# Kernel tuning notes

Measured on AMD Instinct MI355X. Metric: run time of the kernel, lower is better.

Reference implementation:

```python
import jax, jax.numpy as jnp
import numpy as np

# DCE-MRI protocol constants (config values in original repo)
TR = 0.005                      # repetition time (s)
ALPHA = 15.0 / 180.0 * np.pi    # flip angle (rad)
DELTT = 4.5 / 60.0              # temporal resolution (min)
R1_RELAX = 4.5                  # contrast agent relaxivity
SIN_A = float(np.sin(ALPHA))
COS_A = float(np.cos(ALPHA))

B = 262144
T = 112


def setup_inputs() -> dict:
    key = jax.random.key(0)
    k1, k2, k3 = jax.random.split(key, 3)
    param = jax.random.uniform(k1, (B, 3), dtype=jnp.float32)
    T10 = jax.random.uniform(k2, (B, 1), dtype=jnp.float32)
    cp = jax.random.uniform(k3, (B, T), dtype=jnp.float32)
    return {"param": param, "T10": T10, "cp": cp}


def reference(param, T10, cp):
    # Parameter scaling + clamping, as in the torch module
    ktrans = jnp.clip(param[:, 0:1] * 0.2, 1e-5, 0.2)    # [B,1]
    vp = jnp.clip(param[:, 1:2] * 0.1, 0.0005, 0.1)      # [B,1]
    ve = jnp.clip(param[:, 2:3] * 0.6, 0.04, 0.6)        # [B,1]

    # ce[:, t] = sum_{tau<=t} cp[:, tau] * exp(ktrans/ve * (tau - t) * DELTT) * DELTT
    # This exponential convolution is a linear IIR recurrence:
    #   ce[t] = ce[t-1] * exp(-k*DELTT) + cp[t] * DELTT,  k = ktrans/ve
    decay = jnp.exp(-(ktrans / ve)[:, 0] * DELTT)        # [B]

    def step(c, cp_t):
        c = c * decay + cp_t * DELTT
        return c, c

    _, ce_t = jax.lax.scan(step, jnp.zeros(cp.shape[0], dtype=cp.dtype), cp.T)
    ce = ce_t.T * ktrans                                  # [B,T]

    ct = vp * cp + ce                                     # [B,T]
    R1 = 1.0 / T10 + R1_RELAX * ct                        # [B,T]
    E = jnp.exp(-TR * R1)
    s = (1.0 - E) * SIN_A / (1.0 - E * COS_A)
    return s * 20.0
```

## Files before the change

### kernel.cpp

```cpp
#include <hip/hip_runtime.h>


typedef float f32x4 __attribute__((ext_vector_type(4)));

static constexpr int   Bn    = 262144;
static constexpr int   Tn    = 112;
static constexpr int   TT    = 16;
static constexpr int   NT    = Tn / TT;
static constexpr int   LP    = 66;
static constexpr float TRc   = 0.005f;
static constexpr float DELTT = 0.075f;
static constexpr float R1R   = 4.5f;
static constexpr float SIN_A = 0.25881904510252074f;
static constexpr float COS_A = 0.9659258262890683f;

__global__ __launch_bounds__(128) void etofts_kernel(
    const float* __restrict__ param,
    const float* __restrict__ T10,
    const float* __restrict__ cp,
    float* __restrict__ out)
{
    __shared__ float lds[2][TT * LP];

    const int tid = threadIdx.x;
    const int w   = tid >> 6;
    const int l   = tid & 63;
    float* __restrict__ sl = lds[w];

    const int b0 = blockIdx.x * 128 + w * 64;
    const int b  = b0 + l;

    const int rsub = l >> 2;
    const int c4   = l & 3;
    const int tb   = c4 * 4;

    f32x4 r[NT * 4];
    #pragma unroll
    for (int k = 0; k < NT; ++k) {
        #pragma unroll
        for (int i = 0; i < 4; ++i) {
            const int row = i * 16 + rsub;
            r[k * 4 + i] = __builtin_nontemporal_load(
                (const f32x4*)(cp + (size_t)(b0 + row) * Tn + k * TT + c4 * 4));
        }
    }

    const float ktrans = fminf(fmaxf(param[3 * b + 0] * 0.2f, 1e-5f), 0.2f);
    const float vp     = fminf(fmaxf(param[3 * b + 1] * 0.1f, 0.0005f), 0.1f);
    const float ve     = fminf(fmaxf(param[3 * b + 2] * 0.6f, 0.04f), 0.6f);
    const float decay  = __expf(-(ktrans / ve) * DELTT);
    const float r10    = 1.0f / T10[b];

    float c = 0.0f;

    #pragma unroll
    for (int tile = 0; tile < NT; ++tile) {
        #pragma unroll
        for (int i = 0; i < 4; ++i) {
            const int row = i * 16 + rsub;
            const f32x4 v = r[tile * 4 + i];
            sl[(tb + 0) * LP + row] = v.x;
            sl[(tb + 1) * LP + row] = v.y;
            sl[(tb + 2) * LP + row] = v.z;
            sl[(tb + 3) * LP + row] = v.w;
        }

        #pragma unroll
        for (int t = 0; t < TT; ++t) {
            const float cpt = sl[t * LP + l];
            c = fmaf(c, decay, cpt * DELTT);
            const float ct = fmaf(c, ktrans, vp * cpt);
            const float E  = __expf(-TRc * fmaf(R1R, ct, r10));
            sl[t * LP + l] = __fdividef((1.0f - E) * (SIN_A * 20.0f),
                                        fmaf(-E, COS_A, 1.0f));
        }

        #pragma unroll
        for (int i = 0; i < 4; ++i) {
            const int row = i * 16 + rsub;
            f32x4 o;
            o.x = sl[(tb + 0) * LP + row];
            o.y = sl[(tb + 1) * LP + row];
            o.z = sl[(tb + 2) * LP + row];
            o.w = sl[(tb + 3) * LP + row];
            __builtin_nontemporal_store(
                o, (f32x4*)(out + (size_t)(b0 + row) * Tn + tile * TT + c4 * 4));
        }
    }
}

extern "C" void kernel_launch(void* const* d_in, const int* in_sizes, int n_in,
                              void* d_out, int out_size, void* d_ws, size_t ws_size,
                              hipStream_t stream) {
    const float* param = (const float*)d_in[0];
    const float* T10   = (const float*)d_in[1];
    const float* cp    = (const float*)d_in[2];
    float*       out   = (float*)d_out;

    const int threads = 128;
    const int blocks  = Bn / 128;
    etofts_kernel<<<blocks, threads, 0, stream>>>(param, T10, cp, out);
}
```

Measured before the change: 228.3 us.

## Split time recurrence into two halves per row with shuffled carry

```diff
diff --git a/kernel.cpp b/kernel.cpp
--- a/kernel.cpp
+++ b/kernel.cpp
@@ -5,86 +5,105 @@
 
 static constexpr int   Bn    = 262144;
 static constexpr int   Tn    = 112;
-static constexpr int   TT    = 16;
-static constexpr int   NT    = Tn / TT;
-static constexpr int   LP    = 66;
+static constexpr int   Hh    = 56;
+static constexpr int   TTt   = 8;
+static constexpr int   NTt   = 7;
+static constexpr int   LP    = 33;
 static constexpr float TRc   = 0.005f;
 static constexpr float DELTT = 0.075f;
 static constexpr float R1R   = 4.5f;
 static constexpr float SIN_A = 0.25881904510252074f;
 static constexpr float COS_A = 0.9659258262890683f;
 
-__global__ __launch_bounds__(128) void etofts_kernel(
+__global__ __launch_bounds__(256, 8) void etofts_kernel(
     const float* __restrict__ param,
     const float* __restrict__ T10,
     const float* __restrict__ cp,
     float* __restrict__ out)
 {
-    __shared__ float lds[2][TT * LP];
+    __shared__ float lds[4][16 * LP];
 
     const int tid = threadIdx.x;
     const int w   = tid >> 6;
     const int l   = tid & 63;
     float* __restrict__ sl = lds[w];
 
-    const int b0 = blockIdx.x * 128 + w * 64;
-    const int b  = b0 + l;
+    const int r32 = l & 31;
+    const int h   = l >> 5;
+    const int b0  = blockIdx.x * 128 + w * 32;
+    const int row = b0 + r32;
 
-    const int rsub = l >> 2;
-    const int c4   = l & 3;
-    const int tb   = c4 * 4;
+    const float ktrans = fminf(fmaxf(param[3 * row + 0] * 0.2f, 1e-5f), 0.2f);
+    const float vp     = fminf(fmaxf(param[3 * row + 1] * 0.1f, 0.0005f), 0.1f);
+    const float ve     = fminf(fmaxf(param[3 * row + 2] * 0.6f, 0.04f), 0.6f);
+    const float decay  = __expf(-(ktrans / ve) * DELTT);
+    const float r10    = 1.0f / T10[row];
 
-    f32x4 r[NT * 4];
+    const float* half = cp + (size_t)row * Tn + h * Hh;
+    float e = 0.0f;
     #pragma unroll
-    for (int k = 0; k < NT; ++k) {
-        #pragma unroll
-        for (int i = 0; i < 4; ++i) {
-            const int row = i * 16 + rsub;
-            r[k * 4 + i] = __builtin_nontemporal_load(
-                (const f32x4*)(cp + (size_t)(b0 + row) * Tn + k * TT + c4 * 4));
-        }
+    for (int m = 0; m < 14; ++m) {
+        const f32x4 a = *(const f32x4*)(half + 4 * m);
+        e = fmaf(e, decay, a.x * DELTT);
+        e = fmaf(e, decay, a.y * DELTT);
+        e = fmaf(e, decay, a.z * DELTT);
+        e = fmaf(e, decay, a.w * DELTT);
     }
 
-    const float ktrans = fminf(fmaxf(param[3 * b + 0] * 0.2f, 1e-5f), 0.2f);
-    const float vp     = fminf(fmaxf(param[3 * b + 1] * 0.1f, 0.0005f), 0.1f);
-    const float ve     = fminf(fmaxf(param[3 * b + 2] * 0.6f, 0.04f), 0.6f);
-    const float decay  = __expf(-(ktrans / ve) * DELTT);
-    const float r10    = 1.0f / T10[b];
+    const float c55 = __shfl(e, r32);
+    float c = h ? c55 : 0.0f;
 
-    float c = 0.0f;
+    const int rr  = l >> 2;
+    const int p   = l & 3;
+    const int hh  = p >> 1;
+    const int tt0 = (p & 1) * 4;
+
+    f32x4 rb[2];
+    #pragma unroll
+    for (int i = 0; i < 2; ++i)
+        rb[i] = *(const f32x4*)(cp + (size_t)(b0 + i * 16 + rr) * Tn
+                                + hh * Hh + tt0);
 
     #pragma unroll
-    for (int tile = 0; tile < NT; ++tile) {
+    for (int k = 0; k < NTt; ++k) {
         #pragma unroll
-        for (int i = 0; i < 4; ++i) {
-            const int row = i * 16 + rsub;
-            const f32x4 v = r[tile * 4 + i];
-            sl[(tb + 0) * LP + row] = v.x;
-            sl[(tb + 1) * LP + row] = v.y;
-            sl[(tb + 2) * LP + row] = v.z;
-            sl[(tb + 3) * LP + row] = v.w;
+        for (int i = 0; i < 2; ++i) {
+            const int ri = i * 16 + rr;
+            sl[(hh * 8 + tt0 + 0) * LP + ri] = rb[i].x;
+            sl[(hh * 8 + tt0 + 1) * LP + ri] = rb[i].y;
+            sl[(hh * 8 + tt0 + 2) * LP + ri] = rb[i].z;
+            sl[(hh * 8 + tt0 + 3) * LP + ri] = rb[i].w;
+        }
+
+        if (k + 1 < NTt) {
+            #pragma unroll
+            for (int i = 0; i < 2; ++i)
+                rb[i] = *(const f32x4*)(cp + (size_t)(b0 + i * 16 + rr) * Tn
+                                        + hh * Hh + (k + 1) * TTt + tt0);
         }
 
         #pragma unroll
-        for (int t = 0; t < TT; ++t) {
-            const float cpt = sl[t * LP + l];
+        for (int s = 0; s < TTt; ++s) {
+            const int wd  = (h * 8 + s) * LP + r32;
+            const float cpt = sl[wd];
             c = fmaf(c, decay, cpt * DELTT);
             const float ct = fmaf(c, ktrans, vp * cpt);
             const float E  = __expf(-TRc * fmaf(R1R, ct, r10));
-            sl[t * LP + l] = __fdividef((1.0f - E) * (SIN_A * 20.0f),
-                                        fmaf(-E, COS_A, 1.0f));
+            sl[wd] = __fdividef((1.0f - E) * (SIN_A * 20.0f),
+                                fmaf(-E, COS_A, 1.0f));
         }
 
         #pragma unroll
-        for (int i = 0; i < 4; ++i) {
-            const int row = i * 16 + rsub;
+        for (int i = 0; i < 2; ++i) {
+            const int ri = i * 16 + rr;
             f32x4 o;
-            o.x = sl[(tb + 0) * LP + row];
-            o.y = sl[(tb + 1) * LP + row];
-            o.z = sl[(tb + 2) * LP + row];
-            o.w = sl[(tb + 3) * LP + row];
+            o.x = sl[(hh * 8 + tt0 + 0) * LP + ri];
+            o.y = sl[(hh * 8 + tt0 + 1) * LP + ri];
+            o.z = sl[(hh * 8 + tt0 + 2) * LP + ri];
+            o.w = sl[(hh * 8 + tt0 + 3) * LP + ri];
             __builtin_nontemporal_store(
-                o, (f32x4*)(out + (size_t)(b0 + row) * Tn + tile * TT + c4 * 4));
+                o, (f32x4*)(out + (size_t)(b0 + i * 16 + rr) * Tn
+                            + hh * Hh + k * TTt + tt0));
         }
     }
 }
@@ -97,7 +116,7 @@
     const float* cp    = (const float*)d_in[2];
     float*       out   = (float*)d_out;
 
-    const int threads = 128;
+    const int threads = 256;
     const int blocks  = Bn / 128;
     etofts_kernel<<<blocks, threads, 0, stream>>>(param, T10, cp, out);
 }
```

Result: slower. 300.8 us (+31.8%).
